# Kernel optimization log

Hardware: AMD Instinct MI355X
Metric: run time of the kernel (lower is better)

The kernel has to match this reference:

```python
import jax, jax.numpy as jnp
import numpy as np
from jax import lax

B, N, S, K, C = 8, 4096, 1024, 64, 64
RADIUS = 0.2
MLP = [64, 128, 256]
INT_MAX = jnp.iinfo(jnp.int32).max

_batched_gather = jax.vmap(lambda a, i: a[i])  # (N,D),(S,K)->(S,K,D)


def setup_inputs() -> dict:
    key = jax.random.key(0)
    ks = jax.random.split(key, 6)
    xyz = jax.random.uniform(ks[0], (B, N, 3), dtype=jnp.float32)
    points = jax.random.normal(ks[1], (B, N, C), dtype=jnp.float32)
    fps_inds = jax.random.randint(ks[2], (B, S), 0, N, dtype=jnp.int32)
    c_in = [3 + C] + MLP[:-1]
    w0 = jax.random.normal(ks[3], (c_in[0], MLP[0]), dtype=jnp.float32) * 0.1
    w1 = jax.random.normal(ks[4], (c_in[1], MLP[1]), dtype=jnp.float32) * 0.1
    w2 = jax.random.normal(ks[5], (c_in[2], MLP[2]), dtype=jnp.float32) * 0.1
    return {"xyz": xyz, "points": points, "fps_inds": fps_inds,
            "w0": w0, "w1": w1, "w2": w2}


def _query_ball_point(radius, nsample, xyz, new_xyz):
    # dists: (B, S, N)
    dists = jnp.linalg.norm(new_xyz[:, :, None, :] - xyz[:, None, :, :], axis=-1)
    # nsample nearest neighbors (ascending distance), like argsort[:, :, :nsample]
    neg_d, idx = lax.top_k(-dists, nsample)            # (B,S,K)
    valid = (-neg_d) < radius                          # prefix mask (dists ascending)
    idx_m = jnp.where(valid, idx, INT_MAX)
    sidx = jnp.sort(idx_m, axis=-1)
    # invalid slots -> first (smallest) valid index
    return jnp.where(valid, sidx, sidx[:, :, :1])


def reference(xyz, points, fps_inds, w0, w1, w2):
    new_xyz = _batched_gather(xyz, fps_inds)                       # (B,S,3)
    idx = _query_ball_point(RADIUS, K, xyz, new_xyz)               # (B,S,K)
    grouped_xyz = _batched_gather(xyz, idx) - new_xyz[:, :, None]  # (B,S,K,3)
    grouped_pts = _batched_gather(points, idx)                     # (B,S,K,C)
    feat = jnp.concatenate([grouped_xyz, grouped_pts], axis=-1)    # (B,S,K,3+C)
    for w in (w0, w1, w2):  # 1x1 conv == channel matmul, then relu
        feat = jax.nn.relu(jnp.einsum('bskc,cf->bskf', feat, w))
    new_points = jnp.max(feat, axis=2)                             # (B,S,F)
    return new_xyz, new_points
```

## Files before the change

### kernel.cpp

```cpp
#include <hip/hip_runtime.h>

#define NB 8
#define NN 4096
#define NS 1024
#define NC 64
#define OUT_PTS_OFF (NB*NS*3)
#define CAP 512
#define RB 0.2f
#define QPB 4

typedef __attribute__((ext_vector_type(8))) short bf16x8;
typedef __attribute__((ext_vector_type(4))) float f32x4;

static __device__ __forceinline__ short f2bf(float f){
  unsigned u = __float_as_uint(f);
  unsigned r = (u + 0x7FFFu + ((u>>16)&1u)) >> 16;
  return (short)r;
}
static __device__ __forceinline__ float bf2f(short s){
  return __uint_as_float(((unsigned)(unsigned short)s) << 16);
}
static __device__ __forceinline__ unsigned cvtpk(float a, float b){
  unsigned r;
  asm("v_cvt_pk_bf16_f32 %0, %1, %2" : "=v"(r) : "v"(a), "v"(b));
  return r;
}

#define WS_PX1_SH   1048576
#define WS_WF_SH    3145728

__global__ __launch_bounds__(256) void prep_grid(
    const float* __restrict__ w0, const float* __restrict__ w1,
    const float* __restrict__ w2, short* __restrict__ ws,
    const float* __restrict__ xyz, float4* __restrict__ gxyz,
    int* __restrict__ cstart)
{
  __shared__ int hist[125];
  __shared__ int base[125];
  const int tid = threadIdx.x;

  if (blockIdx.x < 184) {
    int e = blockIdx.x*256 + tid;
    if (e >= 47104) return;
    float v = 0.f;
    if (e < 6144) {
      int j=e&7, l=(e>>3)&63, nt=(e>>9)&3, kt=e>>11;
      int k = kt*32 + ((l>>4)<<3) + j, n = nt*16 + (l&15);
      if (k < 64) v = w0[(3+k)*64 + n];
      else if (k < 67) v = w0[(k-64)*64 + n];
    } else if (e < 14336) {
      int e2=e-6144;
      int j=e2&7, l=(e2>>3)&63, nt=(e2>>9)&7, kt=e2>>12;
      int k = kt*32 + ((l>>4)<<3) + j, n = nt*16 + (l&15);
      v = w1[k*128 + n];
    } else {
      int e3=e-14336;
      int j=e3&7, l=(e3>>3)&63, nt=(e3>>9)&15, kt=e3>>13;
      int k = (kt*2 + (j&1))*16 + ((l>>4)<<2) + (j>>1);
      v = w2[k*256 + nt*16 + (l&15)];
    }
    ws[e] = f2bf(v);
    return;
  }

  const int b = blockIdx.x - 184;
  const float* xb = xyz + (size_t)b*NN*3;
  if (tid < 125) hist[tid] = 0;
  __syncthreads();

  float xs[16], ys[16], zs[16]; int cl[16];
  {
    const float4* xv = (const float4*)(xb + tid*48);
    #pragma unroll
    for (int g=0; g<4; ++g) {
      float4 v0 = xv[g*3], v1 = xv[g*3+1], v2 = xv[g*3+2];
      xs[g*4+0]=v0.x; xs[g*4+1]=v0.w; xs[g*4+2]=v1.z; xs[g*4+3]=v2.y;
      ys[g*4+0]=v0.y; ys[g*4+1]=v1.x; ys[g*4+2]=v1.w; ys[g*4+3]=v2.z;
      zs[g*4+0]=v0.z; zs[g*4+1]=v1.y; zs[g*4+2]=v2.x; zs[g*4+3]=v2.w;
    }
  }
  #pragma unroll
  for (int r=0; r<16; ++r) {
    int cx = min(4, (int)(xs[r]*5.0f));
    int cy = min(4, (int)(ys[r]*5.0f));
    int cz = min(4, (int)(zs[r]*5.0f));
    cl[r] = (cz*5+cy)*5+cx;
    atomicAdd(&hist[cl[r]], 1);
  }
  __syncthreads();
  if (tid == 0) {
    int acc = 0;
    for (int c=0; c<125; ++c) { base[c]=acc; cstart[b*128+c]=acc; acc+=hist[c]; }
    cstart[b*128+125] = NN;
  }
  __syncthreads();
  #pragma unroll
  for (int r=0; r<16; ++r) {
    int slot = atomicAdd(&base[cl[r]], 1);
    gxyz[b*NN + slot] = make_float4(xs[r], ys[r], zs[r], __int_as_float(tid*16+r));
  }
}

__global__ __launch_bounds__(256) void px1_select(
    const float* __restrict__ xyz, const float* __restrict__ points,
    const int* __restrict__ fps_inds, const short* __restrict__ wsb,
    const float4* __restrict__ gxyz, const int* __restrict__ cstart,
    short* __restrict__ px1, unsigned short* __restrict__ gsidx,
    float* __restrict__ out)
{
  __shared__ unsigned int cand_d[CAP];
  __shared__ int cand_i[CAP];
  __shared__ int scell[126];
  __shared__ int seg_s[27], seg_b[27], seg_e[27];
  __shared__ int tmp64[64];
  __shared__ int cnt_sh, T_sh;

  const int tid = threadIdx.x;

  if (blockIdx.x < 512) {
    const int w = tid>>6, l = tid&63, lr = l&15, grp = l>>4;
    const int rowbase = blockIdx.x*64 + w*16;
    const int row = rowbase + lr;
    const float* prow = points + (size_t)row*NC;
    const float* xr   = xyz + (size_t)row*3;

    bf16x8 a0, a1, a2;
    {
      float4 u0 = *(const float4*)(prow + grp*8);
      float4 u1 = *(const float4*)(prow + grp*8 + 4);
      float4 u2 = *(const float4*)(prow + 32 + grp*8);
      float4 u3 = *(const float4*)(prow + 32 + grp*8 + 4);
      a0 = (bf16x8){f2bf(u0.x),f2bf(u0.y),f2bf(u0.z),f2bf(u0.w),f2bf(u1.x),f2bf(u1.y),f2bf(u1.z),f2bf(u1.w)};
      a1 = (bf16x8){f2bf(u2.x),f2bf(u2.y),f2bf(u2.z),f2bf(u2.w),f2bf(u3.x),f2bf(u3.y),f2bf(u3.z),f2bf(u3.w)};
      short e0=0,e1=0,e2v=0;
      if (grp==0) { e0=f2bf(xr[0]); e1=f2bf(xr[1]); e2v=f2bf(xr[2]); }
      a2 = (bf16x8){e0,e1,e2v,0,0,0,0,0};
    }
    f32x4 zero4 = {0.f,0.f,0.f,0.f};
    #pragma unroll
    for (int nt=0; nt<4; ++nt) {
      f32x4 acc = zero4;
      bf16x8 b0 = *(const bf16x8*)(wsb + (((0*4+nt)*64 + l)<<3));
      bf16x8 b1 = *(const bf16x8*)(wsb + (((1*4+nt)*64 + l)<<3));
      bf16x8 b2 = *(const bf16x8*)(wsb + (((2*4+nt)*64 + l)<<3));
      acc = __builtin_amdgcn_mfma_f32_16x16x32_bf16(a0, b0, acc, 0,0,0);
      acc = __builtin_amdgcn_mfma_f32_16x16x32_bf16(a1, b1, acc, 0,0,0);
      acc = __builtin_amdgcn_mfma_f32_16x16x32_bf16(a2, b2, acc, 0,0,0);
      #pragma unroll
      for (int i=0;i<4;++i)
        px1[(size_t)(rowbase + grp*4 + i)*64 + nt*16 + lr] = f2bf(acc[i]);
    }
    return;
  }

  const int q = blockIdx.x - 512, b = q >> 10;
  const float* xb = xyz + (size_t)b*NN*3;
  const int fps = fps_inds[q];
  const float qx = xb[fps*3+0], qy = xb[fps*3+1], qz = xb[fps*3+2];
  if (tid < 3) out[q*3+tid] = xb[fps*3+tid];
  if (tid < 126) scell[tid] = cstart[b*128+tid];
  if (tid == 0) cnt_sh = 0;
  __syncthreads();

  if (tid < 32) {
    const int cx = min(4, (int)(qx*5.0f));
    const int cy = min(4, (int)(qy*5.0f));
    const int cz = min(4, (int)(qz*5.0f));
    int len = 0, s = 0;
    if (tid < 27) {
      int ncx = cx + tid%3 - 1, ncy = cy + (tid/3)%3 - 1, ncz = cz + tid/9 - 1;
      if (ncx>=0 && ncx<5 && ncy>=0 && ncy<5 && ncz>=0 && ncz<5) {
        float lox = ncx*0.2f - 1e-5f, hix = lox + 0.2f + 2e-5f;
        float loy = ncy*0.2f - 1e-5f, hiy = loy + 0.2f + 2e-5f;
        float loz = ncz*0.2f - 1e-5f, hiz = loz + 0.2f + 2e-5f;
        float dx = fmaxf(0.f, fmaxf(lox-qx, qx-hix));
        float dy = fmaxf(0.f, fmaxf(loy-qy, qy-hiy));
        float dz = fmaxf(0.f, fmaxf(loz-qz, qz-hiz));
        if (fmaf(dx,dx, fmaf(dy,dy, dz*dz)) <= 0.0402f) {
          int c = (ncz*5+ncy)*5+ncx;
          s = scell[c]; len = scell[c+1] - s;
        }
      }
    }
    int incl = len;
    #pragma unroll
    for (int off=1; off<32; off<<=1) {
      int v = __shfl_up(incl, off, 32);
      if (tid >= off) incl += v;
    }
    if (tid < 27) { seg_s[tid]=s; seg_b[tid]=incl-len; seg_e[tid]=incl; }
    if (tid == 31) T_sh = incl;
  }
  __syncthreads();

  const int T = T_sh;
  const float4* gb = gxyz + b*NN;
  {
    int k = 0;
    for (int t = tid; t < T; t += 256) {
      while (t >= seg_e[k]) ++k;
      float4 p = gb[seg_s[k] + (t - seg_b[k])];
      float fx = qx-p.x, fy = qy-p.y, fz = qz-p.z;
      float ff = fmaf(fx,fx, fmaf(fy,fy, fz*fz));
      if (ff < 0.0402f) {
        float dx=__fsub_rn(qx,p.x), dy=__fsub_rn(qy,p.y), dz=__fsub_rn(qz,p.z);
        float d2=__fadd_rn(__fadd_rn(__fmul_rn(dx,dx),__fmul_rn(dy,dy)),__fmul_rn(dz,dz));
        float d = __fsqrt_rn(d2);
        if (d < RB) {
          int pos = atomicAdd(&cnt_sh, 1);
          if (pos < CAP) { cand_d[pos] = __float_as_uint(d); cand_i[pos] = __float_as_int(p.w); }
        }
      }
    }
  }
  __syncthreads();
  int cnt = cnt_sh; if (cnt > CAP) cnt = CAP;

  if (cnt > 64) {
    for (int j=tid; j<cnt; j+=256) {
      unsigned dj = cand_d[j]; int ij = cand_i[j]; int rk = 0;
      for (int i=0; i<cnt; ++i) {
        unsigned di = cand_d[i];
        rk += (int)((di<dj) | ((di==dj) & (cand_i[i]<ij)));
      }
      if (rk < 64) tmp64[rk] = ij;
    }
    __syncthreads();
    if (tid < 64) {
      int v = tmp64[tid]; int p = 0;
      #pragma unroll
      for (int u=0; u<64; ++u) p += (tmp64[u] < v);
      gsidx[q*64 + p] = (unsigned short)v;
    }
  } else {
    if (tid < cnt) {
      int v = cand_i[tid]; int p = 0;
      for (int u=0; u<cnt; ++u) p += (cand_i[u] < v);
      tmp64[p] = v;
    }
    __syncthreads();
    if (tid < 64) gsidx[q*64 + tid] = (unsigned short)tmp64[tid < cnt ? tid : 0];
  }
}

__global__ __launch_bounds__(256,2) void mlp_kernel(
    const float* __restrict__ xyz, const int* __restrict__ fps_inds,
    const float* __restrict__ w0, const short* __restrict__ wsb,
    const short* __restrict__ px1, const unsigned short* __restrict__ gsidx,
    float* __restrict__ out)
{
  __shared__ __align__(16) short w1s[8192];
  __shared__ __align__(16) short h2f[8192];
  __shared__ float q1s[QPB][64];
  __shared__ int sidx[QPB][64];

  const int tid = threadIdx.x;
  const int w = tid>>6, l = tid&63, lr = l&15, grp = l>>4;
  const int q0 = blockIdx.x*QPB;
  const int b = q0 >> 10;
  const float* xb = xyz + (size_t)b*NN*3;

  bf16x8 b3[4][4];
  #pragma unroll
  for (int kt=0; kt<4; ++kt)
    #pragma unroll
    for (int j=0; j<4; ++j)
      b3[kt][j] = *(const bf16x8*)(wsb + 14336 + (((kt*16 + w*4 + j)*64 + l)<<3));

  #pragma unroll
  for (int e = 0; e < 4; ++e) {
    int s = tid + e*256;
    *(bf16x8*)&w1s[s*8] = *(const bf16x8*)(wsb + 6144 + s*8);
  }
  {
    int qq = tid>>6, t = tid&63;
    int fp = fps_inds[q0+qq];
    sidx[qq][t] = (int)gsidx[(q0+qq)*64 + t];
    q1s[qq][t] = xb[fp*3]*w0[t] + xb[fp*3+1]*w0[64+t] + xb[fp*3+2]*w0[128+t];
  }
  if (tid < QPB*3) {
    int qq = tid/3, c = tid - qq*3;
    int fp = fps_inds[q0+qq];
    out[(q0+qq)*3 + c] = xb[fp*3+c];
  }
  __syncthreads();

  const short* px1b = px1 + (size_t)b*NN*64;
  const int myrow = w*16 + lr;

  bf16x8 v0, v1;
  {
    int idx = sidx[0][myrow];
    v0 = *(const bf16x8*)(px1b + idx*64 + grp*8);
    v1 = *(const bf16x8*)(px1b + idx*64 + 32 + grp*8);
  }

  f32x4 zero4 = {0.f,0.f,0.f,0.f};
  const int uu4 = (lr>>2) << 4;
  const int gg4 = grp << 4;

  for (int qq = 0; qq < QPB; ++qq) {
    if (qq) __syncthreads();

    bf16x8 a20, a21;
    {
      union { unsigned u[4]; bf16x8 v; } ua, ub;
      #pragma unroll
      for (int jp=0; jp<4; ++jp) {
        float x0 = fmaxf(bf2f(v0[2*jp  ]) - q1s[qq][grp*8+2*jp  ], 0.f);
        float x1 = fmaxf(bf2f(v0[2*jp+1]) - q1s[qq][grp*8+2*jp+1], 0.f);
        ua.u[jp] = cvtpk(x0, x1);
        float y0 = fmaxf(bf2f(v1[2*jp  ]) - q1s[qq][32+grp*8+2*jp  ], 0.f);
        float y1 = fmaxf(bf2f(v1[2*jp+1]) - q1s[qq][32+grp*8+2*jp+1], 0.f);
        ub.u[jp] = cvtpk(y0, y1);
      }
      a20 = ua.v; a21 = ub.v;
    }
    if (qq+1 < QPB) {
      int idx = sidx[qq+1][myrow];
      v0 = *(const bf16x8*)(px1b + idx*64 + grp*8);
      v1 = *(const bf16x8*)(px1b + idx*64 + 32 + grp*8);
    }

    #pragma unroll
    for (int ntp=0; ntp<4; ++ntp) {
      f32x4 accA = zero4, accB = zero4;
      bf16x8 bA0 = *(const bf16x8*)&w1s[((0*8 + 2*ntp  )*64 + l)*8];
      bf16x8 bA1 = *(const bf16x8*)&w1s[((1*8 + 2*ntp  )*64 + l)*8];
      bf16x8 bB0 = *(const bf16x8*)&w1s[((0*8 + 2*ntp+1)*64 + l)*8];
      bf16x8 bB1 = *(const bf16x8*)&w1s[((1*8 + 2*ntp+1)*64 + l)*8];
      accA = __builtin_amdgcn_mfma_f32_16x16x32_bf16(a20, bA0, accA, 0,0,0);
      accA = __builtin_amdgcn_mfma_f32_16x16x32_bf16(a21, bA1, accA, 0,0,0);
      accB = __builtin_amdgcn_mfma_f32_16x16x32_bf16(a20, bB0, accB, 0,0,0);
      accB = __builtin_amdgcn_mfma_f32_16x16x32_bf16(a21, bB1, accB, 0,0,0);
      #pragma unroll
      for (int i=0; i<4; ++i) {
        unsigned pv = cvtpk(fmaxf(accA[i],0.f), fmaxf(accB[i],0.f));
        int byteoff = ((((w*4+ntp)*64 + (lr>>2)*16 + grp*4 + i)<<4) + ((lr&3)<<2)) ^ uu4;
        *(unsigned*)((char*)h2f + byteoff) = pv;
      }
    }
    __syncthreads();

    float rm[4][4];
    #pragma unroll
    for (int j=0;j<4;++j)
      #pragma unroll
      for (int i=0;i<4;++i) rm[j][i] = 0.f;
    #pragma unroll
    for (int mt=0; mt<4; ++mt) {
      f32x4 acc[4] = {zero4, zero4, zero4, zero4};
      #pragma unroll
      for (int kt=0; kt<4; ++kt) {
        int byteoff = ((((mt*4+kt)*64 + l)<<4)) ^ gg4;
        bf16x8 a = *(const bf16x8*)((const char*)h2f + byteoff);
        #pragma unroll
        for (int j=0; j<4; ++j)
          acc[j] = __builtin_amdgcn_mfma_f32_16x16x32_bf16(a, b3[kt][j], acc[j], 0,0,0);
      }
      #pragma unroll
      for (int j=0; j<4; ++j)
        #pragma unroll
        for (int i=0; i<4; ++i) rm[j][i] = fmaxf(rm[j][i], acc[j][i]);
    }
    #pragma unroll
    for (int j=0; j<4; ++j) {
      float m = fmaxf(fmaxf(rm[j][0],rm[j][1]), fmaxf(rm[j][2],rm[j][3]));
      m = fmaxf(m, __shfl_xor(m, 16, 64));
      m = fmaxf(m, __shfl_xor(m, 32, 64));
      if (grp == 0) out[OUT_PTS_OFF + (q0+qq)*256 + (w*4+j)*16 + lr] = m;
    }
  }
}

extern "C" void kernel_launch(void* const* d_in, const int* in_sizes, int n_in,
                              void* d_out, int out_size, void* d_ws, size_t ws_size,
                              hipStream_t stream) {
  const float* xyz      = (const float*)d_in[0];
  const float* points   = (const float*)d_in[1];
  const int*   fps_inds = (const int*)d_in[2];
  const float* w0       = (const float*)d_in[3];
  const float* w1       = (const float*)d_in[4];
  const float* w2       = (const float*)d_in[5];
  float* out = (float*)d_out;

  unsigned short* gsidx = (unsigned short*)d_ws;
  float4* gxyz  = (float4*)((char*)d_ws + 1048576);
  int*    cstart= (int*)((char*)d_ws + 1572864);
  short*  px1   = (short*)d_ws + WS_PX1_SH;
  short*  wsb   = (short*)d_ws + WS_WF_SH;

  hipLaunchKernelGGL(prep_grid,  dim3(192), dim3(256), 0, stream,
                     w0, w1, w2, wsb, xyz, gxyz, cstart);
  hipLaunchKernelGGL(px1_select, dim3(512 + NB*NS), dim3(256), 0, stream,
                     xyz, points, fps_inds, wsb, gxyz, cstart, px1, gsidx, out);
  hipLaunchKernelGGL(mlp_kernel, dim3(NB*NS/QPB), dim3(256), 0, stream,
                     xyz, fps_inds, w0, wsb, px1, gsidx, out);
}
```

Baseline: 106.0 us.

## Assign one wavefront per query in ball-query selection with ballot compaction

The neighbour-selection part of px1_select now handles four queries per 256-thread block, one per wavefront, instead of one query per block. Block-wide barriers and the shared atomic counter are replaced by wave barriers and ballot/popcount stream compaction. Distance and index are packed into one 64-bit key so ranking takes a single comparison. The candidate capacity drops from 512 to 256 per query, which could drop in-radius candidates in dense regions and is also a correctness risk, and each query now runs on 64 lanes instead of 256.

```diff
diff --git a/kernel.cpp b/kernel.cpp
--- a/kernel.cpp
+++ b/kernel.cpp
@@ -5,12 +5,13 @@
 #define NS 1024
 #define NC 64
 #define OUT_PTS_OFF (NB*NS*3)
-#define CAP 512
+#define CAP2 256
 #define RB 0.2f
 #define QPB 4
 
 typedef __attribute__((ext_vector_type(8))) short bf16x8;
 typedef __attribute__((ext_vector_type(4))) float f32x4;
+typedef unsigned long long u64;
 
 static __device__ __forceinline__ short f2bf(float f){
   unsigned u = __float_as_uint(f);
@@ -108,12 +109,10 @@
     short* __restrict__ px1, unsigned short* __restrict__ gsidx,
     float* __restrict__ out)
 {
-  __shared__ unsigned int cand_d[CAP];
-  __shared__ int cand_i[CAP];
+  __shared__ u64 candk[4][CAP2];
+  __shared__ int tmpi[4][64];
+  __shared__ int segS[4][28], segB[4][28], segE[4][28];
   __shared__ int scell[126];
-  __shared__ int seg_s[27], seg_b[27], seg_e[27];
-  __shared__ int tmp64[64];
-  __shared__ int cnt_sh, T_sh;
 
   const int tid = threadIdx.x;
 
@@ -153,53 +152,57 @@
     return;
   }
 
-  const int q = blockIdx.x - 512, b = q >> 10;
+  const int sb = blockIdx.x - 512;
+  const int wv = tid>>6, lane = tid&63;
+  const int q = sb*QPB + wv, b = q >> 10;
   const float* xb = xyz + (size_t)b*NN*3;
+
+  if (tid < 126) scell[tid] = cstart[b*128+tid];
+  __syncthreads();
+
   const int fps = fps_inds[q];
   const float qx = xb[fps*3+0], qy = xb[fps*3+1], qz = xb[fps*3+2];
-  if (tid < 3) out[q*3+tid] = xb[fps*3+tid];
-  if (tid < 126) scell[tid] = cstart[b*128+tid];
-  if (tid == 0) cnt_sh = 0;
-  __syncthreads();
-
-  if (tid < 32) {
+  if (lane < 3) out[q*3+lane] = xb[fps*3+lane];
+
+  int len = 0, s = 0;
+  if (lane < 27) {
     const int cx = min(4, (int)(qx*5.0f));
     const int cy = min(4, (int)(qy*5.0f));
     const int cz = min(4, (int)(qz*5.0f));
-    int len = 0, s = 0;
-    if (tid < 27) {
-      int ncx = cx + tid%3 - 1, ncy = cy + (tid/3)%3 - 1, ncz = cz + tid/9 - 1;
-      if (ncx>=0 && ncx<5 && ncy>=0 && ncy<5 && ncz>=0 && ncz<5) {
-        float lox = ncx*0.2f - 1e-5f, hix = lox + 0.2f + 2e-5f;
-        float loy = ncy*0.2f - 1e-5f, hiy = loy + 0.2f + 2e-5f;
-        float loz = ncz*0.2f - 1e-5f, hiz = loz + 0.2f + 2e-5f;
-        float dx = fmaxf(0.f, fmaxf(lox-qx, qx-hix));
-        float dy = fmaxf(0.f, fmaxf(loy-qy, qy-hiy));
-        float dz = fmaxf(0.f, fmaxf(loz-qz, qz-hiz));
-        if (fmaf(dx,dx, fmaf(dy,dy, dz*dz)) <= 0.0402f) {
-          int c = (ncz*5+ncy)*5+ncx;
-          s = scell[c]; len = scell[c+1] - s;
-        }
+    int ncx = cx + lane%3 - 1, ncy = cy + (lane/3)%3 - 1, ncz = cz + lane/9 - 1;
+    if (ncx>=0 && ncx<5 && ncy>=0 && ncy<5 && ncz>=0 && ncz<5) {
+      float lox = ncx*0.2f - 1e-5f, hix = lox + 0.2f + 2e-5f;
+      float loy = ncy*0.2f - 1e-5f, hiy = loy + 0.2f + 2e-5f;
+      float loz = ncz*0.2f - 1e-5f, hiz = loz + 0.2f + 2e-5f;
+      float dx = fmaxf(0.f, fmaxf(lox-qx, qx-hix));
+      float dy = fmaxf(0.f, fmaxf(loy-qy, qy-hiy));
+      float dz = fmaxf(0.f, fmaxf(loz-qz, qz-hiz));
+      if (fmaf(dx,dx, fmaf(dy,dy, dz*dz)) <= 0.0402f) {
+        int c = (ncz*5+ncy)*5+ncx;
+        s = scell[c]; len = scell[c+1] - s;
       }
     }
-    int incl = len;
-    #pragma unroll
-    for (int off=1; off<32; off<<=1) {
-      int v = __shfl_up(incl, off, 32);
-      if (tid >= off) incl += v;
-    }
-    if (tid < 27) { seg_s[tid]=s; seg_b[tid]=incl-len; seg_e[tid]=incl; }
-    if (tid == 31) T_sh = incl;
-  }
-  __syncthreads();
-
-  const int T = T_sh;
+  }
+  int incl = len;
+  #pragma unroll
+  for (int off=1; off<64; off<<=1) {
+    int v = __shfl_up(incl, off, 64);
+    if (lane >= off) incl += v;
+  }
+  const int T = __shfl(incl, 26, 64);
+  if (lane < 27) { segS[wv][lane]=s; segB[wv][lane]=incl-len; segE[wv][lane]=incl; }
+  __builtin_amdgcn_wave_barrier();
+
   const float4* gb = gxyz + b*NN;
-  {
-    int k = 0;
-    for (int t = tid; t < T; t += 256) {
-      while (t >= seg_e[k]) ++k;
-      float4 p = gb[seg_s[k] + (t - seg_b[k])];
+  int base = 0, k = 0;
+  const int rounds = (T + 63) >> 6;
+  const u64 ltmask = (1ull << lane) - 1ull;
+  for (int r = 0; r < rounds; ++r) {
+    int t = r*64 + lane;
+    bool hit = false; u64 key = 0;
+    if (t < T) {
+      while (t >= segE[wv][k]) ++k;
+      float4 p = gb[segS[wv][k] + (t - segB[wv][k])];
       float fx = qx-p.x, fy = qy-p.y, fz = qz-p.z;
       float ff = fmaf(fx,fx, fmaf(fy,fy, fz*fz));
       if (ff < 0.0402f) {
@@ -207,39 +210,41 @@
         float d2=__fadd_rn(__fadd_rn(__fmul_rn(dx,dx),__fmul_rn(dy,dy)),__fmul_rn(dz,dz));
         float d = __fsqrt_rn(d2);
         if (d < RB) {
-          int pos = atomicAdd(&cnt_sh, 1);
-          if (pos < CAP) { cand_d[pos] = __float_as_uint(d); cand_i[pos] = __float_as_int(p.w); }
+          hit = true;
+          key = ((u64)__float_as_uint(d) << 16) | (u64)(unsigned)__float_as_int(p.w);
         }
       }
     }
-  }
-  __syncthreads();
-  int cnt = cnt_sh; if (cnt > CAP) cnt = CAP;
+    u64 m = __ballot(hit);
+    int pos = base + (int)__popcll(m & ltmask);
+    if (hit && pos < CAP2) candk[wv][pos] = key;
+    base += (int)__popcll(m);
+  }
+  int cnt = base < CAP2 ? base : CAP2;
+  __builtin_amdgcn_wave_barrier();
 
   if (cnt > 64) {
-    for (int j=tid; j<cnt; j+=256) {
-      unsigned dj = cand_d[j]; int ij = cand_i[j]; int rk = 0;
-      for (int i=0; i<cnt; ++i) {
-        unsigned di = cand_d[i];
-        rk += (int)((di<dj) | ((di==dj) & (cand_i[i]<ij)));
-      }
-      if (rk < 64) tmp64[rk] = ij;
-    }
-    __syncthreads();
-    if (tid < 64) {
-      int v = tmp64[tid]; int p = 0;
-      #pragma unroll
-      for (int u=0; u<64; ++u) p += (tmp64[u] < v);
-      gsidx[q*64 + p] = (unsigned short)v;
-    }
+    for (int j = lane; j < cnt; j += 64) {
+      u64 kj = candk[wv][j];
+      int rk = 0;
+      for (int i = 0; i < cnt; ++i) rk += (int)(candk[wv][i] < kj);
+      if (rk < 64) tmpi[wv][rk] = (int)(kj & 0xFFFFu);
+    }
+    __builtin_amdgcn_wave_barrier();
+    int v = tmpi[wv][lane];
+    int p = 0;
+    #pragma unroll 8
+    for (int u = 0; u < 64; ++u) p += (int)(tmpi[wv][u] < v);
+    gsidx[q*64 + p] = (unsigned short)v;
   } else {
-    if (tid < cnt) {
-      int v = cand_i[tid]; int p = 0;
-      for (int u=0; u<cnt; ++u) p += (cand_i[u] < v);
-      tmp64[p] = v;
-    }
-    __syncthreads();
-    if (tid < 64) gsidx[q*64 + tid] = (unsigned short)tmp64[tid < cnt ? tid : 0];
+    if (lane < cnt) {
+      int v = (int)(candk[wv][lane] & 0xFFFFu);
+      int p = 0;
+      for (int u = 0; u < cnt; ++u) p += (int)((int)(candk[wv][u] & 0xFFFFu) < v);
+      tmpi[wv][p] = v;
+    }
+    __builtin_amdgcn_wave_barrier();
+    gsidx[q*64 + lane] = (unsigned short)tmpi[wv][lane < cnt ? lane : 0];
   }
 }
 
@@ -392,7 +397,7 @@
 
   hipLaunchKernelGGL(prep_grid,  dim3(192), dim3(256), 0, stream,
                      w0, w1, w2, wsb, xyz, gxyz, cstart);
-  hipLaunchKernelGGL(px1_select, dim3(512 + NB*NS), dim3(256), 0, stream,
+  hipLaunchKernelGGL(px1_select, dim3(512 + NB*NS/QPB), dim3(256), 0, stream,
                      xyz, points, fps_inds, wsb, gxyz, cstart, px1, gsidx, out);
   hipLaunchKernelGGL(mlp_kernel, dim3(NB*NS/QPB), dim3(256), 0, stream,
                      xyz, fps_inds, w0, wsb, px1, gsidx, out);
```

New measurement: 92.24 us (median of 2 runs). 13.0% less time.
